# Kernel tuning notes

Measured on AMD Instinct MI355X. Metric: run time of the kernel, lower is better.

The kernel has to match this reference:

```python
import jax, jax.numpy as jnp
import numpy as np

B, LEADS, T = 256, 12, 2250
ENC_DIM = 768           # encoder.width
LATENT = 128            # latent_dim
K = 512                 # num_embeddings
COMMIT = 0.1            # commitment_cost
IN_DIM = LEADS * T      # 27000


def setup_inputs() -> dict:
    key = jax.random.key(0)
    ks = jax.random.split(key, 9)
    s = lambda d: 1.0 / np.sqrt(d)
    return {
        "x": jax.random.normal(ks[0], (B, LEADS, T), dtype=jnp.float32),
        # frozen pretrained encoder, modeled as a linear projection (stop_gradient in reference)
        "W_enc": jax.random.normal(ks[1], (IN_DIM, ENC_DIM), dtype=jnp.float32) * s(IN_DIM),
        # to_latent
        "W_lat": jax.random.normal(ks[2], (ENC_DIM, LATENT), dtype=jnp.float32) * s(ENC_DIM),
        "b_lat": jnp.zeros((LATENT,), dtype=jnp.float32),
        # VQ codebook: torch.rand - 0.5  -> uniform(-0.5, 0.5)
        "codebook": jax.random.uniform(ks[3], (K, LATENT), dtype=jnp.float32, minval=-0.5, maxval=0.5),
        # decoder: Linear(LATENT, ENC_DIM) -> ReLU -> Linear(ENC_DIM, IN_DIM)
        "W_d1": jax.random.normal(ks[4], (LATENT, ENC_DIM), dtype=jnp.float32) * s(LATENT),
        "b_d1": jnp.zeros((ENC_DIM,), dtype=jnp.float32),
        "W_d2": jax.random.normal(ks[5], (ENC_DIM, IN_DIM), dtype=jnp.float32) * s(ENC_DIM),
        "b_d2": jnp.zeros((IN_DIM,), dtype=jnp.float32),
    }


def _vq(z, codebook):
    # z: [B, D]; codebook: [K, D]
    # distances = |z|^2 + |e|^2 - 2 z e^T   -> [B, K]
    d = (jnp.sum(z * z, axis=1, keepdims=True)
         + jnp.sum(codebook * codebook, axis=1)
         - 2.0 * jnp.matmul(z, codebook.T))
    idx = jnp.argmin(d, axis=1)                 # [B]
    quant = codebook[idx]                       # gather [B, D]
    e_latent = jnp.mean((jax.lax.stop_gradient(quant) - z) ** 2)
    q_latent = jnp.mean((quant - jax.lax.stop_gradient(z)) ** 2)
    loss = q_latent + COMMIT * e_latent
    quant_st = z + jax.lax.stop_gradient(quant - z)   # straight-through
    return quant_st, loss, idx


def reference(x, W_enc, W_lat, b_lat, codebook, W_d1, b_d1, W_d2, b_d2):
    # frozen encoder (requires_grad=False / torch.no_grad)
    features = jax.lax.stop_gradient(x.reshape(x.shape[0], -1) @ W_enc)   # [B, ENC_DIM]
    z = features @ W_lat + b_lat                                          # [B, LATENT]
    z_q, vq_loss, indices = _vq(z, codebook)
    h = jax.nn.relu(z_q @ W_d1 + b_d1)
    x_recon = (h @ W_d2 + b_d2).reshape(-1, LEADS, T)                     # [B, 12, 2250]
    recon_loss = jnp.mean((x_recon - x) ** 2)
    return x_recon, recon_loss + vq_loss, vq_loss, indices
```

## Files before the change

### kernel.cpp

```cpp
#include <hip/hip_runtime.h>
#include <hip/hip_bf16.h>

#define IN_DIM   27000
#define ENC_DIM  768
#define LATENT   128
#define K_CODES  512
#define BATCH    256
#define ZCH      288
#define NZC      94
#define NWC      422
#define BN_R     64
#define NRB      422
#define PADK     40
#define NKT      24

#define OUT_WCTH_US   0
#define OUT_WCTL_US   (128*IN_DIM)
#define OUT_ZPART_F   (128*IN_DIM)

#define WS_Z      0
#define WS_QUANT  (WS_Z + BATCH*LATENT)
#define WS_IDX    (WS_QUANT + BATCH*LATENT)
#define WS_VQPART (WS_IDX + BATCH)
#define WS_RECON  (WS_VQPART + BATCH)
#define WS_HBF    (WS_RECON + 1024)
#define WS_WLH    (WS_HBF + 49152)
#define WS_WLL    (WS_WLH + 49152)

typedef unsigned short ushort_t;
typedef __attribute__((ext_vector_type(4))) float f32x4;
typedef __attribute__((ext_vector_type(8))) short short8x;
typedef __attribute__((ext_vector_type(4))) short short4x;

__device__ __forceinline__ ushort_t bf16_rne(float f) {
    unsigned u = __float_as_uint(f);
    unsigned r = 0x7FFFu + ((u >> 16) & 1u);
    return (ushort_t)((u + r) >> 16);
}
__device__ __forceinline__ void split_f32(float v, ushort_t& h, ushort_t& l) {
    unsigned u  = __float_as_uint(v);
    unsigned uh = u & 0xFFFF0000u;
    h = (ushort_t)(uh >> 16);
    l = bf16_rne(v - __uint_as_float(uh));
}
__device__ __forceinline__ void lds_barrier() {
    asm volatile("s_waitcnt lgkmcnt(0)\n\ts_barrier" ::: "memory");
}

__global__ __launch_bounds__(256) void k_prep(const float* __restrict__ Wlat,
                                              ushort_t* __restrict__ wlh,
                                              ushort_t* __restrict__ wll) {
    const int i4 = blockIdx.x * 256 + threadIdx.x;
    const int k  = i4 >> 5;
    const int n4 = (i4 & 31) * 4;
    float4 v = *(const float4*)(Wlat + (size_t)k * LATENT + n4);
    float vv[4] = {v.x, v.y, v.z, v.w};
#pragma unroll
    for (int j = 0; j < 4; j++) {
        ushort_t h, l;
        split_f32(vv[j], h, l);
        wlh[(size_t)(n4 + j) * ENC_DIM + k] = h;
        wll[(size_t)(n4 + j) * ENC_DIM + k] = l;
    }
}

__global__ __launch_bounds__(256) void k_wc(const float* __restrict__ Wenc,
                                            const ushort_t* __restrict__ wlh,
                                            const ushort_t* __restrict__ wll,
                                            ushort_t* __restrict__ wcth,
                                            ushort_t* __restrict__ wctl) {
    __shared__ ushort_t Bh[2][128][PADK], Bl[2][128][PADK];
    const int t = threadIdx.x, lane = t & 63, w = t >> 6;
    const int lrow = lane & 15, kg = lane >> 4;
    const int m0 = blockIdx.x * 64;
    int arow = m0 + w * 16 + lrow; if (arow > IN_DIM - 1) arow = IN_DIM - 1;
    const float* aptr = Wenc + (size_t)arow * ENC_DIM + kg * 8;
    const int bn = t >> 1, bkc = (t & 1) * 16;
    const size_t bbase = (size_t)bn * ENC_DIM + bkc;

    f32x4 acc[8];
#pragma unroll
    for (int ni = 0; ni < 8; ni++) acc[ni] = (f32x4){0.f, 0.f, 0.f, 0.f};

    float av0[8], av1[8], av2[8], av3[8];
    short8x bh0[2], bl0[2], bh1[2], bl1[2];

#define WC_ALOAD(S, kt)                                                         \
    {                                                                           \
        *(float4*)&av##S[0] = *(const float4*)(aptr + (kt) * 32);               \
        *(float4*)&av##S[4] = *(const float4*)(aptr + (kt) * 32 + 4);           \
    }
#define WC_BLOAD(S, kt)                                                         \
    {                                                                           \
        const ushort_t* ph = wlh + bbase + (kt) * 32;                           \
        const ushort_t* pl = wll + bbase + (kt) * 32;                           \
        bh##S[0] = *(const short8x*)ph;   bh##S[1] = *(const short8x*)(ph + 8); \
        bl##S[0] = *(const short8x*)pl;   bl##S[1] = *(const short8x*)(pl + 8); \
    }
#define WC_BSTORE(S, BI)                                                        \
    {                                                                           \
        *(short8x*)&Bh[BI][bn][bkc]     = bh##S[0];                             \
        *(short8x*)&Bh[BI][bn][bkc + 8] = bh##S[1];                             \
        *(short8x*)&Bl[BI][bn][bkc]     = bl##S[0];                             \
        *(short8x*)&Bl[BI][bn][bkc + 8] = bl##S[1];                             \
    }
#define WC_MFMA(S, BI)                                                          \
    {                                                                           \
        short8x ah, al;                                                         \
        _Pragma("unroll")                                                       \
        for (int i = 0; i < 8; i++) {                                           \
            ushort_t h, l; split_f32(av##S[i], h, l);                           \
            ah[i] = (short)h; al[i] = (short)l;                                 \
        }                                                                       \
        __builtin_amdgcn_s_setprio(1);                                          \
        _Pragma("unroll")                                                       \
        for (int ni = 0; ni < 8; ni++) {                                        \
            short8x bhf = *(const short8x*)&Bh[BI][ni * 16 + lrow][kg * 8];     \
            short8x blf = *(const short8x*)&Bl[BI][ni * 16 + lrow][kg * 8];     \
            acc[ni] = __builtin_amdgcn_mfma_f32_16x16x32_bf16(ah, bhf, acc[ni], 0, 0, 0); \
            acc[ni] = __builtin_amdgcn_mfma_f32_16x16x32_bf16(ah, blf, acc[ni], 0, 0, 0); \
            acc[ni] = __builtin_amdgcn_mfma_f32_16x16x32_bf16(al, bhf, acc[ni], 0, 0, 0); \
        }                                                                       \
        __builtin_amdgcn_s_setprio(0);                                          \
    }

    WC_ALOAD(0, 0) WC_ALOAD(1, 1) WC_ALOAD(2, 2)
    WC_BLOAD(0, 0) WC_BLOAD(1, 1)
    WC_BSTORE(0, 0)
    lds_barrier();

    for (int kt0 = 0; kt0 < NKT; kt0 += 4) {
        if (kt0 + 3 < NKT) WC_ALOAD(3, kt0 + 3)
        if (kt0 + 2 < NKT) WC_BLOAD(0, kt0 + 2)
        WC_MFMA(0, 0)
        if (kt0 + 1 < NKT) WC_BSTORE(1, 1)
        lds_barrier();
        if (kt0 + 4 < NKT) WC_ALOAD(0, kt0 + 4)
        if (kt0 + 3 < NKT) WC_BLOAD(1, kt0 + 3)
        WC_MFMA(1, 1)
        if (kt0 + 2 < NKT) WC_BSTORE(0, 0)
        lds_barrier();
        if (kt0 + 5 < NKT) WC_ALOAD(1, kt0 + 5)
        if (kt0 + 4 < NKT) WC_BLOAD(0, kt0 + 4)
        WC_MFMA(2, 0)
        if (kt0 + 3 < NKT) WC_BSTORE(1, 1)
        lds_barrier();
        if (kt0 + 6 < NKT) WC_ALOAD(2, kt0 + 6)
        if (kt0 + 5 < NKT) WC_BLOAD(1, kt0 + 5)
        WC_MFMA(3, 1)
        if (kt0 + 4 < NKT) WC_BSTORE(0, 0)
        lds_barrier();
    }
#undef WC_ALOAD
#undef WC_BLOAD
#undef WC_BSTORE
#undef WC_MFMA

    const int rowb = m0 + w * 16 + kg * 4;
    if (rowb < IN_DIM) {
#pragma unroll
        for (int ni = 0; ni < 8; ni++) {
            const int col = ni * 16 + lrow;
            short4x h4, l4;
#pragma unroll
            for (int r = 0; r < 4; r++) {
                ushort_t h, l; split_f32(acc[ni][r], h, l);
                h4[r] = (short)h; l4[r] = (short)l;
            }
            *(short4x*)(wcth + (size_t)col * IN_DIM + rowb) = h4;
            *(short4x*)(wctl + (size_t)col * IN_DIM + rowb) = l4;
        }
    }
}

__global__ __launch_bounds__(256) void k_z(const float* __restrict__ x,
                                           const ushort_t* __restrict__ wcth,
                                           const ushort_t* __restrict__ wctl,
                                           float* __restrict__ zpart) {
    __shared__ ushort_t Ah[2][64][PADK], Al[2][64][PADK];
    __shared__ ushort_t Bh[2][128][PADK], Bl[2][128][PADK];
    const int t = threadIdx.x, lane = t & 63, w = t >> 6;
    const int lrow = lane & 15, kg = lane >> 4;
    const int m0 = blockIdx.x * 64;
    const int c  = blockIdx.y;
    const int kb = c * ZCH;
    const int k_end = min(IN_DIM, kb + ZCH);
    const int nt = (k_end - kb + 31) >> 5;

    const int a_row = t >> 3, a_kq = t & 7;
    const int b_n   = t >> 2, b_ck = t & 3;

    float4  areg0[2], areg1[2];
    short8x bhreg0[2], blreg0[2], bhreg1[2], blreg1[2];

    f32x4 acc[8];
#pragma unroll
    for (int ni = 0; ni < 8; ni++) acc[ni] = (f32x4){0.f, 0.f, 0.f, 0.f};

#define Z_LOAD(S, kt)                                                           \
    {                                                                           \
        const int k0_ = kb + (kt) * 32;                                         \
        _Pragma("unroll")                                                       \
        for (int p = 0; p < 2; p++) {                                           \
            const int kk = k0_ + a_kq * 4;                                      \
            if (kk < k_end) {                                                   \
                const int r = m0 + a_row + p * 32;                              \
                areg##S[p] = *(const float4*)(x + (size_t)r * IN_DIM + kk);     \
            } else {                                                            \
                areg##S[p] = (float4){0.f, 0.f, 0.f, 0.f};                      \
            }                                                                   \
        }                                                                       \
        _Pragma("unroll")                                                       \
        for (int p = 0; p < 2; p++) {                                           \
            const int kk = k0_ + b_ck * 8;                                      \
            if (kk < k_end) {                                                   \
                const size_t bo = (size_t)(b_n + p * 64) * IN_DIM + kk;         \
                bhreg##S[p] = *(const short8x*)(wcth + bo);                     \
                blreg##S[p] = *(const short8x*)(wctl + bo);                     \
            } else {                                                            \
                short8x zz = {0, 0, 0, 0, 0, 0, 0, 0};                          \
                bhreg##S[p] = zz; blreg##S[p] = zz;                             \
            }                                                                   \
        }                                                                       \
    }
#define Z_STORE(S, BI)                                                          \
    {                                                                           \
        _Pragma("unroll")                                                       \
        for (int p = 0; p < 2; p++) {                                           \
            const int row = a_row + p * 32;                                     \
            float vv[4] = {areg##S[p].x, areg##S[p].y, areg##S[p].z, areg##S[p].w}; \
            short4x h4, l4;                                                     \
            _Pragma("unroll")                                                   \
            for (int i = 0; i < 4; i++) {                                       \
                ushort_t h, l; split_f32(vv[i], h, l);                          \
                h4[i] = (short)h; l4[i] = (short)l;                             \
            }                                                                   \
            *(short4x*)&Ah[BI][row][a_kq * 4] = h4;                             \
            *(short4x*)&Al[BI][row][a_kq * 4] = l4;                             \
        }                                                                       \
        _Pragma("unroll")                                                       \
        for (int p = 0; p < 2; p++) {                                           \
            const int n = b_n + p * 64;                                         \
            *(short8x*)&Bh[BI][n][b_ck * 8] = bhreg##S[p];                      \
            *(short8x*)&Bl[BI][n][b_ck * 8] = blreg##S[p];                      \
        }                                                                       \
    }
#define Z_MFMA(BI)                                                              \
    {                                                                           \
        short8x ah = *(const short8x*)&Ah[BI][w * 16 + lrow][kg * 8];           \
        short8x al = *(const short8x*)&Al[BI][w * 16 + lrow][kg * 8];           \
        __builtin_amdgcn_s_setprio(1);                                          \
        _Pragma("unroll")                                                       \
        for (int ni = 0; ni < 8; ni++) {                                        \
            short8x bhf = *(const short8x*)&Bh[BI][ni * 16 + lrow][kg * 8];     \
            short8x blf = *(const short8x*)&Bl[BI][ni * 16 + lrow][kg * 8];     \
            acc[ni] = __builtin_amdgcn_mfma_f32_16x16x32_bf16(ah, bhf, acc[ni], 0, 0, 0); \
            acc[ni] = __builtin_amdgcn_mfma_f32_16x16x32_bf16(ah, blf, acc[ni], 0, 0, 0); \
            acc[ni] = __builtin_amdgcn_mfma_f32_16x16x32_bf16(al, bhf, acc[ni], 0, 0, 0); \
        }                                                                       \
        __builtin_amdgcn_s_setprio(0);                                          \
    }

    Z_LOAD(0, 0)
    if (nt > 1) Z_LOAD(1, 1)
    Z_STORE(0, 0)
    lds_barrier();

    for (int kt = 0; kt < nt; kt += 2) {
        if (kt + 2 < nt) Z_LOAD(0, kt + 2)
        Z_MFMA(0)
        if (kt + 1 < nt) Z_STORE(1, 1)
        lds_barrier();
        if (kt + 1 < nt) {
            if (kt + 3 < nt) Z_LOAD(1, kt + 3)
            Z_MFMA(1)
            if (kt + 2 < nt) Z_STORE(0, 0)
            lds_barrier();
        }
    }
#undef Z_LOAD
#undef Z_STORE
#undef Z_MFMA

    float* zp = zpart + (size_t)c * (BATCH * LATENT);
    const int rowb = m0 + w * 16 + kg * 4;
#pragma unroll
    for (int ni = 0; ni < 8; ni++) {
        const int col = ni * 16 + lrow;
#pragma unroll
        for (int r = 0; r < 4; r++)
            zp[(size_t)(rowb + r) * LATENT + col] = acc[ni][r];
    }
}

__global__ __launch_bounds__(256) void k_zred(const float* __restrict__ zpart,
                                              const float* __restrict__ blat,
                                              float* __restrict__ z) {
    const int o = blockIdx.x * 256 + threadIdx.x;
    float s = blat[o & (LATENT - 1)];
    for (int c = 0; c < NZC; c++) s += zpart[(size_t)c * (BATCH * LATENT) + o];
    z[o] = s;
}

__global__ __launch_bounds__(256) void k_vq(const float* __restrict__ z,
                                            const float* __restrict__ cb,
                                            float* __restrict__ quant,
                                            int* __restrict__ idx_out,
                                            float* __restrict__ vqpart) {
    __shared__ float zs[LATENT];
    __shared__ float ds_[256];
    __shared__ int   is_[256];
    const int b = blockIdx.x, t = threadIdx.x;
    if (t < LATENT) zs[t] = z[b * LATENT + t];
    __syncthreads();

    float best_d = 3.4e38f; int best_i = 0;
#pragma unroll
    for (int rep = 0; rep < 2; rep++) {
        const int k = t + rep * 256;
        const float* e = cb + (size_t)k * LATENT;
        float acc = 0.f;
#pragma unroll 4
        for (int d = 0; d < LATENT; d += 4) {
            float4 ev = *(const float4*)(e + d);
            float d0 = zs[d]   - ev.x;
            float d1 = zs[d+1] - ev.y;
            float d2 = zs[d+2] - ev.z;
            float d3 = zs[d+3] - ev.w;
            acc += d0*d0 + d1*d1 + d2*d2 + d3*d3;
        }
        if (acc < best_d) { best_d = acc; best_i = k; }
    }
    ds_[t] = best_d; is_[t] = best_i;
    __syncthreads();
    for (int s = 128; s > 0; s >>= 1) {
        if (t < s) {
            float od = ds_[t+s]; int oi = is_[t+s];
            if (od < ds_[t] || (od == ds_[t] && oi < is_[t])) { ds_[t] = od; is_[t] = oi; }
        }
        __syncthreads();
    }
    const int best = is_[0];
    if (t == 0) idx_out[b] = best;

    float sq = 0.f;
    if (t < LATENT) {
        float q = cb[(size_t)best * LATENT + t];
        quant[b * LATENT + t] = q;
        float dd = q - zs[t];
        sq = dd * dd;
    }
    __syncthreads();
    ds_[t] = sq;
    __syncthreads();
    for (int s = 128; s > 0; s >>= 1) {
        if (t < s) ds_[t] += ds_[t+s];
        __syncthreads();
    }
    if (t == 0) vqpart[b] = ds_[0];
}

__global__ __launch_bounds__(256) void k_h(const float* __restrict__ quant,
                                           const float* __restrict__ Wd1,
                                           const float* __restrict__ bd1,
                                           ushort_t* __restrict__ hfrag) {
    const int bid = blockIdx.x, t = threadIdx.x;
    const int row = bid / 3;
    const int col = (bid % 3) * 256 + t;
    float acc = bd1[col];
    const float* q = quant + row * LATENT;
#pragma unroll 8
    for (int k = 0; k < LATENT; k++)
        acc = fmaf(q[k], Wd1[(size_t)k * ENC_DIM + col], acc);
    const int mt = row >> 4, lrow = row & 15;
    const int kt = col >> 5, kg = (col & 31) >> 3, j = col & 7;
    hfrag[((size_t)(mt * NKT + kt) * 64 + kg * 16 + lrow) * 8 + j] =
        bf16_rne(fmaxf(acc, 0.f));
}

__global__ __launch_bounds__(512) void k_recon_mfma(const ushort_t* __restrict__ hfrag,
                                                    const float* __restrict__ Wd2,
                                                    const float* __restrict__ bd2,
                                                    const float* __restrict__ x,
                                                    float* __restrict__ out,
                                                    float* __restrict__ reconpart) {
    __shared__ ushort_t Bts[2][BN_R][PADK];
    __shared__ float red[512];
    const int t = threadIdx.x, lane = t & 63, wid = t >> 6;
    const int lrow = lane & 15, kg = lane >> 4;
    const int n0 = blockIdx.x * BN_R;

    const int b_n   = lane;
    const int b_kq  = wid;
    const bool bvalid = (n0 + b_n) < IN_DIM;
    const ushort_t* afrag0 = hfrag + ((size_t)(wid * 2 + 0) * NKT * 64 + lane) * 8;
    const ushort_t* afrag1 = hfrag + ((size_t)(wid * 2 + 1) * NKT * 64 + lane) * 8;

    f32x4 acc[2][4];
#pragma unroll
    for (int mi = 0; mi < 2; mi++)
#pragma unroll
        for (int ni = 0; ni < 4; ni++) acc[mi][ni] = (f32x4){0.f, 0.f, 0.f, 0.f};

    short8x a0[2], a1[2], a2[2], a3[2];
    float   bregs0[4], bregs1[4], bregs2[4], bregs3[4];

#define R_ALOAD(S, kt)                                                          \
    {                                                                           \
        a##S[0] = *(const short8x*)(afrag0 + (size_t)(kt) * 512);               \
        a##S[1] = *(const short8x*)(afrag1 + (size_t)(kt) * 512);               \
    }
#define R_BLOAD(S, kt)                                                          \
    {                                                                           \
        if (bvalid) {                                                           \
            const float* wp = Wd2 + (size_t)((kt) * 32 + b_kq * 4) * IN_DIM + n0 + b_n; \
            _Pragma("unroll")                                                   \
            for (int j = 0; j < 4; j++) bregs##S[j] = wp[(size_t)j * IN_DIM];   \
        } else {                                                                \
            _Pragma("unroll")                                                   \
            for (int j = 0; j < 4; j++) bregs##S[j] = 0.f;                      \
        }                                                                       \
    }
#define R_BSTORE(S, BI)                                                         \
    {                                                                           \
        short4x bb;                                                             \
        _Pragma("unroll")                                                       \
        for (int j = 0; j < 4; j++) bb[j] = (short)bf16_rne(bregs##S[j]);       \
        *(short4x*)&Bts[BI][b_n][b_kq * 4] = bb;                                \
    }
#define R_MFMA(S, BI)                                                           \
    {                                                                           \
        short8x b_[4];                                                          \
        _Pragma("unroll")                                                       \
        for (int ni = 0; ni < 4; ni++)                                          \
            b_[ni] = *(const short8x*)&Bts[BI][ni * 16 + lrow][kg * 8];         \
        __builtin_amdgcn_s_setprio(1);                                          \
        _Pragma("unroll")                                                       \
        for (int mi = 0; mi < 2; mi++)                                          \
            _Pragma("unroll")                                                   \
            for (int ni = 0; ni < 4; ni++)                                      \
                acc[mi][ni] = __builtin_amdgcn_mfma_f32_16x16x32_bf16(a##S[mi], b_[ni], acc[mi][ni], 0, 0, 0); \
        __builtin_amdgcn_s_setprio(0);                                          \
    }

    R_ALOAD(0, 0) R_BLOAD(0, 0)
    R_ALOAD(1, 1) R_BLOAD(1, 1)
    R_ALOAD(2, 2) R_BLOAD(2, 2)
    R_BSTORE(0, 0)
    lds_barrier();

    for (int kt0 = 0; kt0 < NKT; kt0 += 4) {
        if (kt0 + 3 < NKT) { R_ALOAD(3, kt0 + 3) R_BLOAD(3, kt0 + 3) }
        R_MFMA(0, 0)
        if (kt0 + 1 < NKT) R_BSTORE(1, 1)
        lds_barrier();
        if (kt0 + 4 < NKT) { R_ALOAD(0, kt0 + 4) R_BLOAD(0, kt0 + 4) }
        R_MFMA(1, 1)
        if (kt0 + 2 < NKT) R_BSTORE(2, 0)
        lds_barrier();
        if (kt0 + 5 < NKT) { R_ALOAD(1, kt0 + 5) R_BLOAD(1, kt0 + 5) }
        R_MFMA(2, 0)
        if (kt0 + 3 < NKT) R_BSTORE(3, 1)
        lds_barrier();
        if (kt0 + 6 < NKT) { R_ALOAD(2, kt0 + 6) R_BLOAD(2, kt0 + 6) }
        R_MFMA(3, 1)
        if (kt0 + 4 < NKT) R_BSTORE(0, 0)
        lds_barrier();
    }
#undef R_ALOAD
#undef R_BLOAD
#undef R_BSTORE
#undef R_MFMA

    float lsq = 0.f;
#pragma unroll
    for (int mi = 0; mi < 2; mi++) {
        const int rowb = wid * 32 + mi * 16 + kg * 4;
#pragma unroll
        for (int ni = 0; ni < 4; ni++) {
            const int col = n0 + ni * 16 + lrow;
            if (col < IN_DIM) {
                const float bb = bd2[col];
#pragma unroll
                for (int r = 0; r < 4; r++) {
                    const int row = rowb + r;
                    float v = acc[mi][ni][r] + bb;
                    float e = v - x[(size_t)row * IN_DIM + col];
                    lsq += e * e;
                    out[(size_t)row * IN_DIM + col] = v;
                }
            }
        }
    }

    red[t] = lsq;
    __syncthreads();
    for (int s = 256; s > 0; s >>= 1) {
        if (t < s) red[t] += red[t + s];
        __syncthreads();
    }
    if (t == 0) reconpart[blockIdx.x] = red[0];
}

__global__ __launch_bounds__(256) void k_final(const float* __restrict__ reconpart,
                                               const float* __restrict__ vqpart,
                                               const int* __restrict__ idx,
                                               float* __restrict__ out,
                                               long long obase) {
    __shared__ float red[256];
    const int t = threadIdx.x;
    float s = 0.f;
    for (int i = t; i < NRB; i += 256) s += reconpart[i];
    red[t] = s;
    __syncthreads();
    for (int st = 128; st > 0; st >>= 1) {
        if (t < st) red[t] += red[t + st];
        __syncthreads();
    }
    const float recon_sum = red[0];
    __syncthreads();
    red[t] = vqpart[t];
    __syncthreads();
    for (int st = 128; st > 0; st >>= 1) {
        if (t < st) red[t] += red[t + st];
        __syncthreads();
    }
    const float vq_sum = red[0];
    if (t == 0) {
        float recon_loss = recon_sum / (float)((size_t)BATCH * IN_DIM);
        float vq_loss = 1.1f * vq_sum / (float)(BATCH * LATENT);
        out[obase + 0] = recon_loss + vq_loss;
        out[obase + 1] = vq_loss;
    }
    out[obase + 2 + t] = (float)idx[t];
}

extern "C" void kernel_launch(void* const* d_in, const int* in_sizes, int n_in,
                              void* d_out, int out_size, void* d_ws, size_t ws_size,
                              hipStream_t stream) {
    int ix = 0, iwe = 1, iwl = 2, ibl = 3, icb = 4, iwd1 = 5, ibd1 = 6, iwd2 = 7, ibd2 = 8;
    if (n_in == 9 && in_sizes[0] != BATCH * IN_DIM) {
        int p20[2] = {1, 7}, n20 = 0, p98[2] = {2, 5}, n98 = 0;
        for (int i = 0; i < 9; i++) {
            const int s = in_sizes[i];
            if      (s == BATCH * IN_DIM)    ix = i;
            else if (s == LATENT)            ibl = i;
            else if (s == K_CODES * LATENT)  icb = i;
            else if (s == ENC_DIM)           ibd1 = i;
            else if (s == IN_DIM)            ibd2 = i;
            else if (s == IN_DIM * ENC_DIM)  { if (n20 < 2) p20[n20++] = i; }
            else if (s == ENC_DIM * LATENT)  { if (n98 < 2) p98[n98++] = i; }
        }
        iwd2 = p20[0]; iwe = p20[1];
        iwd1 = p98[0]; iwl = p98[1];
    }
    const float* x    = (const float*)d_in[ix];
    const float* Wenc = (const float*)d_in[iwe];
    const float* Wlat = (const float*)d_in[iwl];
    const float* blat = (const float*)d_in[ibl];
    const float* cb   = (const float*)d_in[icb];
    const float* Wd1  = (const float*)d_in[iwd1];
    const float* bd1  = (const float*)d_in[ibd1];
    const float* Wd2  = (const float*)d_in[iwd2];
    const float* bd2  = (const float*)d_in[ibd2];

    float* out = (float*)d_out;
    ushort_t* wcth  = (ushort_t*)d_out + OUT_WCTH_US;
    ushort_t* wctl  = (ushort_t*)d_out + OUT_WCTL_US;
    float*    zpart = out + OUT_ZPART_F;

    float* ws            = (float*)d_ws;
    float* z             = ws + WS_Z;
    float* quant         = ws + WS_QUANT;
    int*   idxp          = (int*)(ws + WS_IDX);
    float* vqpart        = ws + WS_VQPART;
    float* reconpart     = ws + WS_RECON;
    ushort_t* hfrag      = (ushort_t*)(ws + WS_HBF);
    ushort_t* wlh        = (ushort_t*)(ws + WS_WLH);
    ushort_t* wll        = (ushort_t*)(ws + WS_WLL);

    const long long obase = (long long)out_size - 258;

    k_prep      <<<96, 256, 0, stream>>>(Wlat, wlh, wll);
    k_wc        <<<NWC, 256, 0, stream>>>(Wenc, wlh, wll, wcth, wctl);
    k_z         <<<dim3(4, NZC), 256, 0, stream>>>(x, wcth, wctl, zpart);
    k_zred      <<<128, 256, 0, stream>>>(zpart, blat, z);
    k_vq        <<<BATCH, 256, 0, stream>>>(z, cb, quant, idxp, vqpart);
    k_h         <<<768, 256, 0, stream>>>(quant, Wd1, bd1, hfrag);
    k_recon_mfma<<<NRB, 512, 0, stream>>>(hfrag, Wd2, bd2, x, out, reconpart);
    k_final     <<<1, 256, 0, stream>>>(reconpart, vqpart, idxp, out, obase);
}
```

Measured before the change: 129.9 us.

## Double tile width in k_wc and k_recon_mfma to share B-tile staging

k_wc now processes 128 rows per block with 512 threads, so the staged W_lat B tile in LDS is shared by twice as many waves and global B loads per block are spread over more threads. k_recon_mfma widens its N tile from 64 to 128 columns, holding 2x8 accumulators per wave and loading 8 W_d2 rows per thread, which halves block count and the redundant A-fragment loads. This trades fewer blocks (211 on a large GPU) and higher register pressure for better reuse, which may lower occupancy and tail balance.

```diff
diff --git a/kernel.cpp b/kernel.cpp
--- a/kernel.cpp
+++ b/kernel.cpp
@@ -8,9 +8,9 @@
 #define BATCH    256
 #define ZCH      288
 #define NZC      94
-#define NWC      422
-#define BN_R     64
-#define NRB      422
+#define NWC      211
+#define BN_R     128
+#define NRB      211
 #define PADK     40
 #define NKT      24
 
@@ -64,18 +64,19 @@
     }
 }
 
-__global__ __launch_bounds__(256) void k_wc(const float* __restrict__ Wenc,
+__global__ __launch_bounds__(512) void k_wc(const float* __restrict__ Wenc,
                                             const ushort_t* __restrict__ wlh,
                                             const ushort_t* __restrict__ wll,
                                             ushort_t* __restrict__ wcth,
                                             ushort_t* __restrict__ wctl) {
     __shared__ ushort_t Bh[2][128][PADK], Bl[2][128][PADK];
-    const int t = threadIdx.x, lane = t & 63, w = t >> 6;
+    const int t = threadIdx.x, lane = t & 63, wid = t >> 6;
     const int lrow = lane & 15, kg = lane >> 4;
-    const int m0 = blockIdx.x * 64;
-    int arow = m0 + w * 16 + lrow; if (arow > IN_DIM - 1) arow = IN_DIM - 1;
+    const int half = wid >> 2, w8 = wid & 3;
+    const int m0 = blockIdx.x * 128;
+    int arow = m0 + half * 64 + w8 * 16 + lrow; if (arow > IN_DIM - 1) arow = IN_DIM - 1;
     const float* aptr = Wenc + (size_t)arow * ENC_DIM + kg * 8;
-    const int bn = t >> 1, bkc = (t & 1) * 16;
+    const int bn = t >> 2, bkc = (t & 3) * 8;
     const size_t bbase = (size_t)bn * ENC_DIM + bkc;
 
     f32x4 acc[8];
@@ -83,7 +84,7 @@
     for (int ni = 0; ni < 8; ni++) acc[ni] = (f32x4){0.f, 0.f, 0.f, 0.f};
 
     float av0[8], av1[8], av2[8], av3[8];
-    short8x bh0[2], bl0[2], bh1[2], bl1[2];
+    short8x bh0, bl0, bh1, bl1;
 
 #define WC_ALOAD(S, kt)                                                         \
     {                                                                           \
@@ -92,17 +93,13 @@
     }
 #define WC_BLOAD(S, kt)                                                         \
     {                                                                           \
-        const ushort_t* ph = wlh + bbase + (kt) * 32;                           \
-        const ushort_t* pl = wll + bbase + (kt) * 32;                           \
-        bh##S[0] = *(const short8x*)ph;   bh##S[1] = *(const short8x*)(ph + 8); \
-        bl##S[0] = *(const short8x*)pl;   bl##S[1] = *(const short8x*)(pl + 8); \
+        bh##S = *(const short8x*)(wlh + bbase + (kt) * 32);                     \
+        bl##S = *(const short8x*)(wll + bbase + (kt) * 32);                     \
     }
 #define WC_BSTORE(S, BI)                                                        \
     {                                                                           \
-        *(short8x*)&Bh[BI][bn][bkc]     = bh##S[0];                             \
-        *(short8x*)&Bh[BI][bn][bkc + 8] = bh##S[1];                             \
-        *(short8x*)&Bl[BI][bn][bkc]     = bl##S[0];                             \
-        *(short8x*)&Bl[BI][bn][bkc + 8] = bl##S[1];                             \
+        *(short8x*)&Bh[BI][bn][bkc] = bh##S;                                    \
+        *(short8x*)&Bl[BI][bn][bkc] = bl##S;                                    \
     }
 #define WC_MFMA(S, BI)                                                          \
     {                                                                           \
@@ -156,7 +153,7 @@
 #undef WC_BSTORE
 #undef WC_MFMA
 
-    const int rowb = m0 + w * 16 + kg * 4;
+    const int rowb = m0 + half * 64 + w8 * 16 + kg * 4;
     if (rowb < IN_DIM) {
 #pragma unroll
         for (int ni = 0; ni < 8; ni++) {
@@ -390,20 +387,20 @@
     const int lrow = lane & 15, kg = lane >> 4;
     const int n0 = blockIdx.x * BN_R;
 
-    const int b_n   = lane;
-    const int b_kq  = wid;
+    const int b_n   = t & 127;
+    const int b_kq  = t >> 7;
     const bool bvalid = (n0 + b_n) < IN_DIM;
     const ushort_t* afrag0 = hfrag + ((size_t)(wid * 2 + 0) * NKT * 64 + lane) * 8;
     const ushort_t* afrag1 = hfrag + ((size_t)(wid * 2 + 1) * NKT * 64 + lane) * 8;
 
-    f32x4 acc[2][4];
+    f32x4 acc[2][8];
 #pragma unroll
     for (int mi = 0; mi < 2; mi++)
 #pragma unroll
-        for (int ni = 0; ni < 4; ni++) acc[mi][ni] = (f32x4){0.f, 0.f, 0.f, 0.f};
+        for (int ni = 0; ni < 8; ni++) acc[mi][ni] = (f32x4){0.f, 0.f, 0.f, 0.f};
 
     short8x a0[2], a1[2], a2[2], a3[2];
-    float   bregs0[4], bregs1[4], bregs2[4], bregs3[4];
+    float   bregs0[8], bregs1[8], bregs2[8], bregs3[8];
 
 #define R_ALOAD(S, kt)                                                          \
     {                                                                           \
@@ -413,33 +410,30 @@
 #define R_BLOAD(S, kt)                                                          \
     {                                                                           \
         if (bvalid) {                                                           \
-            const float* wp = Wd2 + (size_t)((kt) * 32 + b_kq * 4) * IN_DIM + n0 + b_n; \
+            const float* wp = Wd2 + (size_t)((kt) * 32 + b_kq * 8) * IN_DIM + n0 + b_n; \
             _Pragma("unroll")                                                   \
-            for (int j = 0; j < 4; j++) bregs##S[j] = wp[(size_t)j * IN_DIM];   \
+            for (int j = 0; j < 8; j++) bregs##S[j] = wp[(size_t)j * IN_DIM];   \
         } else {                                                                \
             _Pragma("unroll")                                                   \
-            for (int j = 0; j < 4; j++) bregs##S[j] = 0.f;                      \
+            for (int j = 0; j < 8; j++) bregs##S[j] = 0.f;                      \
         }                                                                       \
     }
 #define R_BSTORE(S, BI)                                                         \
     {                                                                           \
-        short4x bb;                                                             \
-        _Pragma("unroll")                                                       \
-        for (int j = 0; j < 4; j++) bb[j] = (short)bf16_rne(bregs##S[j]);       \
-        *(short4x*)&Bts[BI][b_n][b_kq * 4] = bb;                                \
+        short8x bb;                                                             \
+        _Pragma("unroll")                                                       \
+        for (int j = 0; j < 8; j++) bb[j] = (short)bf16_rne(bregs##S[j]);       \
+        *(short8x*)&Bts[BI][b_n][b_kq * 8] = bb;                                \
     }
 #define R_MFMA(S, BI)                                                           \
     {                                                                           \
-        short8x b_[4];                                                          \
-        _Pragma("unroll")                                                       \
-        for (int ni = 0; ni < 4; ni++)                                          \
-            b_[ni] = *(const short8x*)&Bts[BI][ni * 16 + lrow][kg * 8];         \
         __builtin_amdgcn_s_setprio(1);                                          \
         _Pragma("unroll")                                                       \
-        for (int mi = 0; mi < 2; mi++)                                          \
-            _Pragma("unroll")                                                   \
-            for (int ni = 0; ni < 4; ni++)                                      \
-                acc[mi][ni] = __builtin_amdgcn_mfma_f32_16x16x32_bf16(a##S[mi], b_[ni], acc[mi][ni], 0, 0, 0); \
+        for (int ni = 0; ni < 8; ni++) {                                        \
+            short8x b_ = *(const short8x*)&Bts[BI][ni * 16 + lrow][kg * 8];     \
+            acc[0][ni] = __builtin_amdgcn_mfma_f32_16x16x32_bf16(a##S[0], b_, acc[0][ni], 0, 0, 0); \
+            acc[1][ni] = __builtin_amdgcn_mfma_f32_16x16x32_bf16(a##S[1], b_, acc[1][ni], 0, 0, 0); \
+        }                                                                       \
         __builtin_amdgcn_s_setprio(0);                                          \
     }
 
@@ -477,7 +471,7 @@
     for (int mi = 0; mi < 2; mi++) {
         const int rowb = wid * 32 + mi * 16 + kg * 4;
 #pragma unroll
-        for (int ni = 0; ni < 4; ni++) {
+        for (int ni = 0; ni < 8; ni++) {
             const int col = n0 + ni * 16 + lrow;
             if (col < IN_DIM) {
                 const float bb = bd2[col];
@@ -582,7 +576,7 @@
     const long long obase = (long long)out_size - 258;
 
     k_prep      <<<96, 256, 0, stream>>>(Wlat, wlh, wll);
-    k_wc        <<<NWC, 256, 0, stream>>>(Wenc, wlh, wll, wcth, wctl);
+    k_wc        <<<NWC, 512, 0, stream>>>(Wenc, wlh, wll, wcth, wctl);
     k_z         <<<dim3(4, NZC), 256, 0, stream>>>(x, wcth, wctl, zpart);
     k_zred      <<<128, 256, 0, stream>>>(zpart, blat, z);
     k_vq        <<<BATCH, 256, 0, stream>>>(z, cb, quant, idxp, vqpart);
```

Measured after the change: 127.5 us. No clear change (-1.8%).
